# Performance work log

Hardware: AMD Instinct MI355X
Metric: run time of the kernel (lower is better)

Reference implementation:

```python
import jax, jax.numpy as jnp
import numpy as np

D_MODEL = 1024
N_HEADS = 16
HEAD_DIM = D_MODEL // N_HEADS


def setup_inputs() -> dict:
    key = jax.random.key(0)
    k_x, k_wqkv, k_bqkv, k_wp, k_bp = jax.random.split(key, 5)
    B, N = 2, 2048
    x = jax.random.normal(k_x, (B, N, D_MODEL), dtype=jnp.float32)
    s = 1.0 / np.sqrt(D_MODEL)
    w_qkv = jax.random.uniform(k_wqkv, (D_MODEL, 3 * D_MODEL), jnp.float32, -s, s)
    b_qkv = jax.random.uniform(k_bqkv, (3 * D_MODEL,), jnp.float32, -s, s)
    w_proj = jax.random.uniform(k_wp, (D_MODEL, D_MODEL), jnp.float32, -s, s)
    b_proj = jax.random.uniform(k_bp, (D_MODEL,), jnp.float32, -s, s)
    return {"x": x, "w_qkv": w_qkv, "b_qkv": b_qkv, "w_proj": w_proj, "b_proj": b_proj}


def reference(x, w_qkv, b_qkv, w_proj, b_proj):
    B, N, C = x.shape
    scale = HEAD_DIM ** (-0.5)
    qkv = x @ w_qkv + b_qkv  # [B, N, 3C]
    qkv = qkv.reshape(B, N, 3, N_HEADS, HEAD_DIM).transpose(2, 0, 3, 1, 4)
    q, k, v = qkv[0], qkv[1], qkv[2]  # each [B, H, N, Dh]
    p = jnp.einsum('bhnd,bhmd->bhnm', q, k) * scale  # [B, H, N, N]
    p = jax.nn.softmax(p, axis=-1)
    o = jnp.einsum('bhnm,bhmd->bhnd', p, v)  # [B, H, N, Dh]
    o = o.transpose(0, 2, 1, 3).reshape(B, N, C)
    return o @ w_proj + b_proj
```

## Files before the change

kernel.cpp:

```cpp
#include <hip/hip_runtime.h>


typedef short v8s __attribute__((ext_vector_type(8)));
typedef float v4f __attribute__((ext_vector_type(4)));
typedef unsigned int v4u __attribute__((ext_vector_type(4)));

#define QSCALE 0.18033688011112042f

#if defined(__has_builtin)
# if __has_builtin(__builtin_amdgcn_exp2f)
#  define EXP2(x) __builtin_amdgcn_exp2f(x)
# endif
#endif
#ifndef EXP2
static __device__ __forceinline__ float exp2_asm(float x) {
    float r;
    asm volatile("v_exp_f32 %0, %1\n\ts_nop 1" : "=v"(r) : "v"(x));
    return r;
}
# define EXP2(x) exp2_asm(x)
#endif

static __device__ __forceinline__ unsigned short f2bf_fast(float f) {
    union { float f; unsigned int u; } a;
    a.f = f;
    return (unsigned short)((a.u + 0x8000u) >> 16);
}

static __device__ __forceinline__ unsigned int pack_bf16(float lo, float hi) {
    union { float f; unsigned int u; } a, b;
    a.f = lo; b.f = hi;
    return __builtin_amdgcn_perm(b.u + 0x8000u, a.u + 0x8000u, 0x07060302u);
}

#define GLD16(g, l) __builtin_amdgcn_global_load_lds( \
    (const __attribute__((address_space(1))) unsigned int*)(g), \
    (__attribute__((address_space(3))) unsigned int*)(l), 16, 0, 0)

__global__ __launch_bounds__(256) void prep(const float* __restrict__ x,
                                            unsigned short* __restrict__ xb,
                                            const float* __restrict__ w_qkv,
                                            unsigned short* __restrict__ wqkvt,
                                            const float* __restrict__ w_proj,
                                            unsigned short* __restrict__ wprojt) {
    __shared__ float tile[32][33];
    const int bid = blockIdx.x, tid = threadIdx.x;
    if (bid < 4096) {
        int i = bid * 256 + tid;
        float4 f = ((const float4*)x)[i];
        ushort4 o;
        o.x = f2bf_fast(f.x); o.y = f2bf_fast(f.y); o.z = f2bf_fast(f.z); o.w = f2bf_fast(f.w);
        ((ushort4*)xb)[i] = o;
        return;
    }
    const float* w; unsigned short* wt; int R, C, bx, by;
    if (bid < 7168) { w = w_qkv; wt = wqkvt; R = 1024; C = 3072;
                      int t = bid - 4096; bx = t % 96; by = t / 96; }
    else            { w = w_proj; wt = wprojt; R = 1024; C = 1024;
                      int t = bid - 7168; bx = t & 31; by = t >> 5; }
    const int tx = tid & 31, ty = tid >> 5;
    const int c0 = bx * 32, r0 = by * 32;
#pragma unroll
    for (int j = 0; j < 32; j += 8)
        tile[ty + j][tx] = w[(r0 + ty + j) * C + c0 + tx];
    __syncthreads();
#pragma unroll
    for (int j = 0; j < 32; j += 8)
        wt[(c0 + ty + j) * R + r0 + tx] = f2bf_fast(tile[tx][ty + j]);
}

__global__ __launch_bounds__(256) void gemm_bt(const unsigned short* __restrict__ A,
                                               const unsigned short* __restrict__ Bt,
                                               const float* __restrict__ bias,
                                               int M, int N, int K, int mode,
                                               unsigned short* __restrict__ qo,
                                               unsigned short* __restrict__ ko,
                                               unsigned short* __restrict__ vto,
                                               float* __restrict__ outp) {
    __shared__ unsigned short Sh[24576];
    const int tid = threadIdx.x;
    const int wave = tid >> 6, lane = tid & 63;
    const int quad = lane >> 4, l16 = lane & 15;
    const int W = gridDim.x;
    const int id = blockIdx.y * W + blockIdx.x;
    const int s = (id & 7) * (W << 2) + (id >> 3);
    const int bm = (s / W) * 128, bn = (s % W) * 128;
    const int wm = (wave >> 1) * 64, wn = (wave & 1) * 64;
    const int rsw = (quad ^ ((l16 >> 1) & 3)) << 3;

    v4f acc[4][4];
#pragma unroll
    for (int i = 0; i < 4; i++)
#pragma unroll
        for (int j = 0; j < 4; j++) acc[i][j] = (v4f){0.f, 0.f, 0.f, 0.f};

#define GSTAGE(off, kk) do { \
    _Pragma("unroll") \
    for (int i_ = 0; i_ < 2; i_++) { \
        int c_ = i_ * 256 + tid; \
        int r_ = c_ >> 2; \
        int g_ = ((c_ & 3) ^ ((r_ >> 1) & 3)) << 3; \
        GLD16(&A[(bm + r_) * K + (kk) + g_], &Sh[(off) + (c_ << 3)]); \
        GLD16(&Bt[(bn + r_) * K + (kk) + g_], &Sh[(off) + 4096 + (c_ << 3)]); \
    } } while (0)

#define GCOMP(off) do { \
    v8s af_[4], bf_[4]; \
    _Pragma("unroll") \
    for (int mi_ = 0; mi_ < 4; mi_++) \
        af_[mi_] = *(const v8s*)&Sh[(off) + (wm + mi_ * 16 + l16) * 32 + rsw]; \
    _Pragma("unroll") \
    for (int ni_ = 0; ni_ < 4; ni_++) \
        bf_[ni_] = *(const v8s*)&Sh[(off) + 4096 + (wn + ni_ * 16 + l16) * 32 + rsw]; \
    _Pragma("unroll") \
    for (int mi_ = 0; mi_ < 4; mi_++) \
        _Pragma("unroll") \
        for (int ni_ = 0; ni_ < 4; ni_++) \
            acc[mi_][ni_] = __builtin_amdgcn_mfma_f32_16x16x32_bf16( \
                af_[mi_], bf_[ni_], acc[mi_][ni_], 0, 0, 0); \
    } while (0)

    const int nt = K >> 5;
    int o0 = 0, o1 = 8192, o2 = 16384;
    GSTAGE(o0, 0);
    GSTAGE(o1, 32);
    for (int t = 0; t < nt - 1; ++t) {
        asm volatile("s_waitcnt vmcnt(4)" ::: "memory");
        __builtin_amdgcn_s_barrier();
        __builtin_amdgcn_sched_barrier(0);
        if (t + 2 < nt) GSTAGE(o2, (t + 2) << 5);
        GCOMP(o0);
        int tmp = o0; o0 = o1; o1 = o2; o2 = tmp;
    }
    asm volatile("s_waitcnt vmcnt(0)" ::: "memory");
    __builtin_amdgcn_s_barrier();
    __builtin_amdgcn_sched_barrier(0);
    GCOMP(o0);
#undef GSTAGE
#undef GCOMP

    if (mode == 1) {
#pragma unroll
        for (int mi = 0; mi < 4; mi++)
#pragma unroll
            for (int ni = 0; ni < 4; ni++) {
                int col = bn + wn + ni * 16 + l16;
                float bv = bias[col];
                int row0 = bm + wm + mi * 16 + quad * 4;
#pragma unroll
                for (int r = 0; r < 4; r++)
                    outp[(row0 + r) * N + col] = acc[mi][ni][r] + bv;
            }
    } else if (bn < 2048) {
        const int isq = (bn < 1024);
        unsigned short* dst = isq ? qo : ko;
        const float sc = isq ? QSCALE : 1.0f;
        __syncthreads();
#pragma unroll
        for (int mi = 0; mi < 4; mi++)
#pragma unroll
            for (int ni = 0; ni < 4; ni++) {
                int c = wn + ni * 16 + l16;
                float bv = bias[bn + c];
                int r0 = wm + mi * 16 + quad * 4;
#pragma unroll
                for (int r = 0; r < 4; r++)
                    Sh[(r0 + r) * 136 + c] = f2bf_fast((acc[mi][ni][r] + bv) * sc);
            }
        __syncthreads();
        const int bb = bm >> 11, nb = bm & 2047;
#pragma unroll
        for (int j = 0; j < 8; j++) {
            int idx = j * 256 + tid;
            int r = idx >> 4, c8 = idx & 15;
            int rem = (bn + c8 * 8) & 1023;
            int h = rem >> 6, dh = rem & 63;
            *(int4*)&dst[(((bb * 16 + h) << 11) + nb + r) * 64 + dh] =
                *(const int4*)&Sh[r * 136 + c8 * 8];
        }
    } else {
        __syncthreads();
#pragma unroll
        for (int mi = 0; mi < 4; mi++)
#pragma unroll
            for (int ni = 0; ni < 4; ni++) {
                int col = bn + wn + ni * 16 + l16;
                float bv = bias[col];
                ushort4 pk;
                pk.x = f2bf_fast(acc[mi][ni][0] + bv);
                pk.y = f2bf_fast(acc[mi][ni][1] + bv);
                pk.z = f2bf_fast(acc[mi][ni][2] + bv);
                pk.w = f2bf_fast(acc[mi][ni][3] + bv);
                *(ushort4*)&Sh[(wn + ni * 16 + l16) * 136 +
                               wm + ((mi >> 1) * 32) + quad * 8 + ((mi & 1) * 4)] = pk;
            }
        __syncthreads();
        const int b = bm >> 11, n_base = bm & 2047;
#pragma unroll
        for (int j = 0; j < 8; j++) {
            int idx = j * 256 + tid;
            int Lcol = idx >> 4, rc = idx & 15;
            int rem = (bn + Lcol) & 1023;
            int h = rem >> 6, dh = rem & 63;
            *(int4*)&vto[((((b * 16 + h) * 64 + dh) << 11) + n_base + rc * 8)] =
                *(const int4*)&Sh[Lcol * 136 + rc * 8];
        }
    }
}

__global__ __launch_bounds__(256, 2) void attn(const unsigned short* __restrict__ q,
                                               const unsigned short* __restrict__ k,
                                               const unsigned short* __restrict__ vt,
                                               unsigned short* __restrict__ o) {
    __shared__ unsigned short KsF[2 * 4096];
    __shared__ unsigned short VsF[4 * 4096];
    const int tid = threadIdx.x;
    const int wave = tid >> 6, lane = tid & 63;
    const int quad = lane >> 4, l16 = lane & 15;
    const int sw = l16 & 7;

    const int id = blockIdx.y * 16 + blockIdx.x;
    const int bh = (id & 7) * 4 + ((id >> 3) & 3);
    const int wq0 = (id >> 5) * 128 + wave * 32;
    const int rowg = bh * 2048 + wq0;

    v8s qf[2][2];
#pragma unroll
    for (int g = 0; g < 2; g++)
#pragma unroll
        for (int half = 0; half < 2; half++)
            qf[g][half] = *(const v8s*)&q[(rowg + g * 16 + l16) * 64 + half * 32 + quad * 8];

    v8s onef;
#pragma unroll
    for (int j = 0; j < 8; j++) onef[j] = (short)0x3F80;

    v4f oacc[2][4];
    v4f lacc[2];
#pragma unroll
    for (int g = 0; g < 2; g++) {
        lacc[g] = (v4f){0.f, 0.f, 0.f, 0.f};
#pragma unroll
        for (int dt = 0; dt < 4; dt++) oacc[g][dt] = (v4f){0.f, 0.f, 0.f, 0.f};
    }

    const unsigned short* kbase = k + (((long)bh << 11) * 64);
    const unsigned short* vbase = vt + (((long)bh * 64) << 11);

#define STAGE(ko, vo, n0s) do { \
    _Pragma("unroll") \
    for (int i_ = 0; i_ < 2; i_++) { \
        int c_ = i_ * 256 + tid; \
        int r_ = c_ >> 3; \
        int chs_ = ((c_ & 7) ^ (r_ & 7)) << 3; \
        GLD16(&kbase[((n0s) + r_) * 64 + chs_], &KsF[(ko) + (c_ << 3)]); \
        GLD16(&vbase[(r_ << 11) + (n0s) + chs_], &VsF[(vo) + (c_ << 3)]); \
    } } while (0)

#define WAITB() do { asm volatile("s_waitcnt vmcnt(0)" ::: "memory"); \
    __builtin_amdgcn_s_barrier(); __builtin_amdgcn_sched_barrier(0); } while (0)

    auto QK = [&](const unsigned short* Kc, v4f (&sreg)[2][4]) {
#pragma unroll
        for (int ni = 0; ni < 4; ni++) {
            int rowk = (ni * 16 + l16) * 64;
            v8s kf0 = *(const v8s*)&Kc[rowk + ((quad ^ sw) << 3)];
            v8s kf1 = *(const v8s*)&Kc[rowk + (((4 + quad) ^ sw) << 3)];
#pragma unroll
            for (int g = 0; g < 2; g++) {
                v4f z = (v4f){0.f, 0.f, 0.f, 0.f};
                z = __builtin_amdgcn_mfma_f32_16x16x32_bf16(kf0, qf[g][0], z, 0, 0, 0);
                z = __builtin_amdgcn_mfma_f32_16x16x32_bf16(kf1, qf[g][1], z, 0, 0, 0);
                sreg[g][ni] = z;
            }
        }
    };
    auto EXPP = [&](v4f (&sreg)[2][4], v8s (&af)[2][2]) {
#pragma unroll
        for (int g = 0; g < 2; g++)
#pragma unroll
            for (int t = 0; t < 2; t++) {
                v4u w;
                w[0] = pack_bf16(EXP2(sreg[g][2 * t][0]),     EXP2(sreg[g][2 * t][1]));
                w[1] = pack_bf16(EXP2(sreg[g][2 * t][2]),     EXP2(sreg[g][2 * t][3]));
                w[2] = pack_bf16(EXP2(sreg[g][2 * t + 1][0]), EXP2(sreg[g][2 * t + 1][1]));
                w[3] = pack_bf16(EXP2(sreg[g][2 * t + 1][2]), EXP2(sreg[g][2 * t + 1][3]));
                union { v4u u; v8s s8; } cv;
                cv.u = w;
                af[g][t] = cv.s8;
            }
    };
    auto PV = [&](v8s (&af)[2][2], const unsigned short* Vc) {
#pragma unroll
        for (int dt = 0; dt < 4; dt++) {
            int rowv = (dt * 16 + l16) * 64;
            v8s vf0 = *(const v8s*)&Vc[rowv + ((quad ^ sw) << 3)];
            v8s vf1 = *(const v8s*)&Vc[rowv + (((4 + quad) ^ sw) << 3)];
#pragma unroll
            for (int g = 0; g < 2; g++) {
                oacc[g][dt] = __builtin_amdgcn_mfma_f32_16x16x32_bf16(af[g][0], vf0, oacc[g][dt], 0, 0, 0);
                oacc[g][dt] = __builtin_amdgcn_mfma_f32_16x16x32_bf16(af[g][1], vf1, oacc[g][dt], 0, 0, 0);
            }
        }
#pragma unroll
        for (int g = 0; g < 2; g++) {
            lacc[g] = __builtin_amdgcn_mfma_f32_16x16x32_bf16(af[g][0], onef, lacc[g], 0, 0, 0);
            lacc[g] = __builtin_amdgcn_mfma_f32_16x16x32_bf16(af[g][1], onef, lacc[g], 0, 0, 0);
        }
    };

    v4f sA[2][4], sB[2][4];
    v8s afA[2][2], afB[2][2];

    STAGE(0, 0, 0);
    WAITB();
    QK(KsF, sA);
    STAGE(4096, 4096, 64);

    for (int i = 1; i < 31; i += 2) {
        WAITB();
        __builtin_amdgcn_s_setprio(1);
        EXPP(sA, afA);
        QK(KsF + 4096, sB);
        PV(afA, VsF + (((i - 1) & 3) << 12));
        __builtin_amdgcn_s_setprio(0);
        STAGE(0, ((i + 1) & 3) << 12, (i + 1) * 64);

        WAITB();
        __builtin_amdgcn_s_setprio(1);
        EXPP(sB, afB);
        QK(KsF, sA);
        PV(afB, VsF + ((i & 3) << 12));
        __builtin_amdgcn_s_setprio(0);
        STAGE(4096, ((i + 2) & 3) << 12, (i + 2) * 64);
    }

    WAITB();
    __builtin_amdgcn_s_setprio(1);
    EXPP(sA, afA);
    QK(KsF + 4096, sB);
    PV(afA, VsF + ((30 & 3) << 12));
    EXPP(sB, afB);
    PV(afB, VsF + ((31 & 3) << 12));
    __builtin_amdgcn_s_setprio(0);
#undef STAGE
#undef WAITB

    const int b = bh >> 4, h = bh & 15;
#pragma unroll
    for (int g = 0; g < 2; g++)
#pragma unroll
        for (int r = 0; r < 4; r++) {
            float linv = 1.0f / lacc[g][r];
            int n = wq0 + g * 16 + quad * 4 + r;
#pragma unroll
            for (int dt = 0; dt < 4; dt++)
                o[(b * 2048 + n) * 1024 + h * 64 + dt * 16 + l16] =
                    f2bf_fast(oacc[g][dt][r] * linv);
        }
}

extern "C" void kernel_launch(void* const* d_in, const int* in_sizes, int n_in,
                              void* d_out, int out_size, void* d_ws, size_t ws_size,
                              hipStream_t stream) {
    const float* x      = (const float*)d_in[0];
    const float* w_qkv  = (const float*)d_in[1];
    const float* b_qkv  = (const float*)d_in[2];
    const float* w_proj = (const float*)d_in[3];
    const float* b_proj = (const float*)d_in[4];
    float* outp = (float*)d_out;

    unsigned short* ws     = (unsigned short*)d_ws;
    unsigned short* xb     = ws;
    unsigned short* wqkvt  = ws + 4194304;
    unsigned short* wprojt = wqkvt + 3145728;
    unsigned short* qws    = wprojt + 1048576;
    unsigned short* kws    = qws + 4194304;
    unsigned short* vtws   = kws + 4194304;
    unsigned short* ows    = xb;

    prep<<<8192, 256, 0, stream>>>(x, xb, w_qkv, wqkvt, w_proj, wprojt);
    gemm_bt<<<dim3(24, 32), 256, 0, stream>>>(xb, wqkvt, b_qkv, 4096, 3072, 1024, 0,
                                              qws, kws, vtws, nullptr);
    attn<<<dim3(16, 32), 256, 0, stream>>>(qws, kws, vtws, ows);
    gemm_bt<<<dim3(8, 32), 256, 0, stream>>>(ows, wprojt, b_proj, 4096, 1024, 1024, 1,
                                             nullptr, nullptr, nullptr, outp);
}
```

Baseline: 173.0 us.

## Unroll GEMM triple-buffer loop and issue attention prefetch before compute

The GEMM main loop is unrolled by three so buffer offsets become compile-time constants, with the peeled last iterations written out explicitly. This hardcodes K to 1024. The attention loop is fully unrolled into 31 phases, and the next K/V tile's global-to-LDS load is now issued right after the barrier instead of after the compute. The goal is to overlap more of the load latency with the exp/MFMA work. The cost is larger code size, and K and V buffers are reused with a tighter margin, which carries a possible hazard on buffer overwrite timing.

```diff
diff --git a/kernel.cpp b/kernel.cpp
--- a/kernel.cpp
+++ b/kernel.cpp
@@ -120,22 +120,30 @@
                 af_[mi_], bf_[ni_], acc[mi_][ni_], 0, 0, 0); \
     } while (0)
 
-    const int nt = K >> 5;
-    int o0 = 0, o1 = 8192, o2 = 16384;
-    GSTAGE(o0, 0);
-    GSTAGE(o1, 32);
-    for (int t = 0; t < nt - 1; ++t) {
-        asm volatile("s_waitcnt vmcnt(4)" ::: "memory");
-        __builtin_amdgcn_s_barrier();
-        __builtin_amdgcn_sched_barrier(0);
-        if (t + 2 < nt) GSTAGE(o2, (t + 2) << 5);
-        GCOMP(o0);
-        int tmp = o0; o0 = o1; o1 = o2; o2 = tmp;
+#define GSTEP(boff, soff, t) do { \
+    asm volatile("s_waitcnt vmcnt(4)" ::: "memory"); \
+    __builtin_amdgcn_s_barrier(); \
+    __builtin_amdgcn_sched_barrier(0); \
+    GSTAGE(soff, ((t) + 2) << 5); \
+    GCOMP(boff); \
+} while (0)
+
+    GSTAGE(0, 0);
+    GSTAGE(8192, 32);
+    for (int t = 0; t < 30; t += 3) {
+        GSTEP(0,     16384, t);
+        GSTEP(8192,  0,     t + 1);
+        GSTEP(16384, 8192,  t + 2);
     }
+    asm volatile("s_waitcnt vmcnt(4)" ::: "memory");
+    __builtin_amdgcn_s_barrier();
+    __builtin_amdgcn_sched_barrier(0);
+    GCOMP(0);
     asm volatile("s_waitcnt vmcnt(0)" ::: "memory");
     __builtin_amdgcn_s_barrier();
     __builtin_amdgcn_sched_barrier(0);
-    GCOMP(o0);
+    GCOMP(8192);
+#undef GSTEP
 #undef GSTAGE
 #undef GCOMP
 
@@ -260,7 +268,7 @@
 #define WAITB() do { asm volatile("s_waitcnt vmcnt(0)" ::: "memory"); \
     __builtin_amdgcn_s_barrier(); __builtin_amdgcn_sched_barrier(0); } while (0)
 
-    auto QK = [&](const unsigned short* Kc, v4f (&sreg)[2][4]) {
+    auto QK = [&](const unsigned short* Kc, v4f (&sr)[2][4]) {
 #pragma unroll
         for (int ni = 0; ni < 4; ni++) {
             int rowk = (ni * 16 + l16) * 64;
@@ -271,26 +279,26 @@
                 v4f z = (v4f){0.f, 0.f, 0.f, 0.f};
                 z = __builtin_amdgcn_mfma_f32_16x16x32_bf16(kf0, qf[g][0], z, 0, 0, 0);
                 z = __builtin_amdgcn_mfma_f32_16x16x32_bf16(kf1, qf[g][1], z, 0, 0, 0);
-                sreg[g][ni] = z;
+                sr[g][ni] = z;
             }
         }
     };
-    auto EXPP = [&](v4f (&sreg)[2][4], v8s (&af)[2][2]) {
+    auto EXPP = [&](v4f (&sr)[2][4], v8s (&afr)[2][2]) {
 #pragma unroll
         for (int g = 0; g < 2; g++)
 #pragma unroll
             for (int t = 0; t < 2; t++) {
                 v4u w;
-                w[0] = pack_bf16(EXP2(sreg[g][2 * t][0]),     EXP2(sreg[g][2 * t][1]));
-                w[1] = pack_bf16(EXP2(sreg[g][2 * t][2]),     EXP2(sreg[g][2 * t][3]));
-                w[2] = pack_bf16(EXP2(sreg[g][2 * t + 1][0]), EXP2(sreg[g][2 * t + 1][1]));
-                w[3] = pack_bf16(EXP2(sreg[g][2 * t + 1][2]), EXP2(sreg[g][2 * t + 1][3]));
+                w[0] = pack_bf16(EXP2(sr[g][2 * t][0]),     EXP2(sr[g][2 * t][1]));
+                w[1] = pack_bf16(EXP2(sr[g][2 * t][2]),     EXP2(sr[g][2 * t][3]));
+                w[2] = pack_bf16(EXP2(sr[g][2 * t + 1][0]), EXP2(sr[g][2 * t + 1][1]));
+                w[3] = pack_bf16(EXP2(sr[g][2 * t + 1][2]), EXP2(sr[g][2 * t + 1][3]));
                 union { v4u u; v8s s8; } cv;
                 cv.u = w;
-                af[g][t] = cv.s8;
+                afr[g][t] = cv.s8;
             }
     };
-    auto PV = [&](v8s (&af)[2][2], const unsigned short* Vc) {
+    auto PV = [&](v8s (&afr)[2][2], const unsigned short* Vc) {
 #pragma unroll
         for (int dt = 0; dt < 4; dt++) {
             int rowv = (dt * 16 + l16) * 64;
@@ -298,51 +306,46 @@
             v8s vf1 = *(const v8s*)&Vc[rowv + (((4 + quad) ^ sw) << 3)];
 #pragma unroll
             for (int g = 0; g < 2; g++) {
-                oacc[g][dt] = __builtin_amdgcn_mfma_f32_16x16x32_bf16(af[g][0], vf0, oacc[g][dt], 0, 0, 0);
-                oacc[g][dt] = __builtin_amdgcn_mfma_f32_16x16x32_bf16(af[g][1], vf1, oacc[g][dt], 0, 0, 0);
+                oacc[g][dt] = __builtin_amdgcn_mfma_f32_16x16x32_bf16(afr[g][0], vf0, oacc[g][dt], 0, 0, 0);
+                oacc[g][dt] = __builtin_amdgcn_mfma_f32_16x16x32_bf16(afr[g][1], vf1, oacc[g][dt], 0, 0, 0);
             }
         }
 #pragma unroll
         for (int g = 0; g < 2; g++) {
-            lacc[g] = __builtin_amdgcn_mfma_f32_16x16x32_bf16(af[g][0], onef, lacc[g], 0, 0, 0);
-            lacc[g] = __builtin_amdgcn_mfma_f32_16x16x32_bf16(af[g][1], onef, lacc[g], 0, 0, 0);
+            lacc[g] = __builtin_amdgcn_mfma_f32_16x16x32_bf16(afr[g][0], onef, lacc[g], 0, 0, 0);
+            lacc[g] = __builtin_amdgcn_mfma_f32_16x16x32_bf16(afr[g][1], onef, lacc[g], 0, 0, 0);
         }
     };
 
-    v4f sA[2][4], sB[2][4];
-    v8s afA[2][2], afB[2][2];
+    v4f sreg[2][2][4];
+    v8s af[2][2];
+
+#define PHASE(T) do { \
+    WAITB(); \
+    if ((T) < 31) STAGE(((((T) + 1) & 1) * 4096), ((((T) + 1) & 3) * 4096), (((T) + 1) * 64)); \
+    __builtin_amdgcn_s_setprio(1); \
+    EXPP(sreg[((T) + 1) & 1], af); \
+    QK(KsF + ((T) & 1) * 4096, sreg[(T) & 1]); \
+    PV(af, VsF + ((((T) + 3) & 3) * 4096)); \
+    __builtin_amdgcn_s_setprio(0); \
+} while (0)
 
     STAGE(0, 0, 0);
     WAITB();
-    QK(KsF, sA);
     STAGE(4096, 4096, 64);
-
-    for (int i = 1; i < 31; i += 2) {
-        WAITB();
-        __builtin_amdgcn_s_setprio(1);
-        EXPP(sA, afA);
-        QK(KsF + 4096, sB);
-        PV(afA, VsF + (((i - 1) & 3) << 12));
-        __builtin_amdgcn_s_setprio(0);
-        STAGE(0, ((i + 1) & 3) << 12, (i + 1) * 64);
-
-        WAITB();
-        __builtin_amdgcn_s_setprio(1);
-        EXPP(sB, afB);
-        QK(KsF, sA);
-        PV(afB, VsF + ((i & 3) << 12));
-        __builtin_amdgcn_s_setprio(0);
-        STAGE(4096, ((i + 2) & 3) << 12, (i + 2) * 64);
-    }
-
-    WAITB();
+    QK(KsF, sreg[0]);
+
+    PHASE(1);  PHASE(2);  PHASE(3);  PHASE(4);  PHASE(5);  PHASE(6);
+    PHASE(7);  PHASE(8);  PHASE(9);  PHASE(10); PHASE(11); PHASE(12);
+    PHASE(13); PHASE(14); PHASE(15); PHASE(16); PHASE(17); PHASE(18);
+    PHASE(19); PHASE(20); PHASE(21); PHASE(22); PHASE(23); PHASE(24);
+    PHASE(25); PHASE(26); PHASE(27); PHASE(28); PHASE(29); PHASE(30);
+    PHASE(31);
     __builtin_amdgcn_s_setprio(1);
-    EXPP(sA, afA);
-    QK(KsF + 4096, sB);
-    PV(afA, VsF + ((30 & 3) << 12));
-    EXPP(sB, afB);
-    PV(afB, VsF + ((31 & 3) << 12));
+    EXPP(sreg[1], af);
+    PV(af, VsF + 3 * 4096);
     __builtin_amdgcn_s_setprio(0);
+#undef PHASE
 #undef STAGE
 #undef WAITB
 
```

New measurement: 166.7 us. 3.6% less time.
